# Kernel tuning notes

Hardware: AMD Instinct MI355X
Metric: run time of the kernel (lower is better)

## Reference

```python
import jax, jax.numpy as jnp
import numpy as np

N, DIN, DOUT, K, R = 4096, 256, 256, 3, 3
DENSITY = 0.005  # ~20 neighbors per node


def setup_inputs() -> dict:
    key = jax.random.key(0)
    ks = jax.random.split(key, 6)
    x = jax.random.normal(ks[0], (N, DIN), dtype=jnp.float32)
    supports = (jax.random.uniform(ks[1], (K, N, N)) < DENSITY).astype(jnp.int32)
    atten_supports = (jax.random.uniform(ks[2], (R, N, N)) < DENSITY).astype(jnp.int32)
    # torch Linear default init ~ U(-1/sqrt(fan_in), 1/sqrt(fan_in)); scaled normal is fine
    W_t = jax.random.normal(ks[3], (K, DIN, DOUT), dtype=jnp.float32) / np.sqrt(DIN).astype(np.float32)
    W_l = jax.random.normal(ks[4], (K, R + 1, DOUT), dtype=jnp.float32) / np.sqrt(DOUT).astype(np.float32)
    W_r = jax.random.normal(ks[5], (K, R + 1, DOUT), dtype=jnp.float32) / np.sqrt(DOUT).astype(np.float32)
    return {"x": x, "supports": supports, "atten_supports": atten_supports,
            "W_t": W_t, "W_l": W_l, "W_r": W_r}


def reference(x, supports, atten_supports, W_t, W_l, W_r):
    NEG = jnp.float32(-1e30)  # finite stand-in for -inf; exp(NEG - max) == 0 in fp32
    amask = (atten_supports != 0).astype(x.dtype)  # [R, N, N]
    out = None
    for k in range(K):
        wx = x @ W_t[k]                      # [N, Dout]
        al = wx @ W_l[k].T                   # [N, R+1] all left attention scalars
        ar = wx @ W_r[k].T                   # [N, R+1]
        # sum_i mask_i * (al_i[row] + ar_i[col]) without R dense [N,N] temps
        scores = (jnp.einsum('rnm,nr->nm', amask, al[:, :R])
                  + jnp.einsum('rnm,mr->nm', amask, ar[:, :R]))
        smask = (supports[k] != 0).astype(x.dtype)  # [N, N]
        scores = scores + smask * (al[:, R][:, None] + ar[:, R][None, :])
        # masked_fill(scores == 0, -inf) -> softmax -> NaN rows (no edges) -> 0
        valid = scores != 0
        probs = jax.nn.softmax(jnp.where(valid, scores, NEG), axis=-1)
        probs = jnp.where(valid.any(axis=-1, keepdims=True), probs, jnp.float32(0.0))
        out_k = probs @ wx                   # [N, Dout]
        out = out_k if out is None else out + out_k
    return jax.nn.elu(out)
```

## Files before the change

kernel.cpp:

```cpp
#include <hip/hip_runtime.h>
#include <hip/hip_bf16.h>
#include <math.h>

#define N 4096
#define DIN 256
#define DOUT 256
#define KK 3
#define CAP 512

typedef int i4 __attribute__((ext_vector_type(4)));

__global__ __launch_bounds__(256) void gemm_wx(const float* __restrict__ x,
                                               const float* __restrict__ Wt,
                                               float* __restrict__ wx) {
    __shared__ float As[16][68];
    __shared__ float Bs[16][68];
    const int k  = blockIdx.z;
    const int n0 = blockIdx.y * 64;
    const int d0 = blockIdx.x * 64;
    const int tx = threadIdx.x, ty = threadIdx.y;
    const int t  = ty * 16 + tx;
    float acc[4][4] = {};
    const float* xA = x + (size_t)(n0 + (t >> 2)) * DIN + ((t & 3) * 4);
    const float* wB = Wt + (size_t)k * DIN * DOUT + (size_t)(t >> 4) * DOUT + d0 + (t & 15) * 4;
    for (int k0 = 0; k0 < DIN; k0 += 16) {
        float4 xa = *(const float4*)(xA + k0);
        float4 wb = *(const float4*)(wB + (size_t)k0 * DOUT);
        const int r = t >> 2, c = (t & 3) * 4;
        As[c + 0][r] = xa.x; As[c + 1][r] = xa.y; As[c + 2][r] = xa.z; As[c + 3][r] = xa.w;
        *(float4*)&Bs[t >> 4][(t & 15) * 4] = wb;
        __syncthreads();
#pragma unroll
        for (int kk = 0; kk < 16; ++kk) {
            float4 a = *(const float4*)&As[kk][ty * 4];
            float4 b = *(const float4*)&Bs[kk][tx * 4];
            float av[4] = {a.x, a.y, a.z, a.w};
            float bv[4] = {b.x, b.y, b.z, b.w};
#pragma unroll
            for (int i = 0; i < 4; ++i)
#pragma unroll
                for (int j = 0; j < 4; ++j)
                    acc[i][j] = fmaf(av[i], bv[j], acc[i][j]);
        }
        __syncthreads();
    }
#pragma unroll
    for (int i = 0; i < 4; ++i) {
        const int row = n0 + ty * 4 + i;
        float4 o = {acc[i][0], acc[i][1], acc[i][2], acc[i][3]};
        *(float4*)(wx + ((size_t)k * N + row) * DOUT + d0 + tx * 4) = o;
    }
}

__global__ __launch_bounds__(256) void alar_kernel(const float* __restrict__ wx,
                                                   const float* __restrict__ Wl,
                                                   const float* __restrict__ Wr,
                                                   float* __restrict__ al,
                                                   float* __restrict__ ar) {
    const int k    = blockIdx.y;
    const int wid  = threadIdx.x >> 6;
    const int lane = threadIdx.x & 63;
    const int n    = blockIdx.x * 4 + wid;
    float4 wxv = *(const float4*)(wx + ((size_t)k * N + n) * DOUT + lane * 4);
#pragma unroll
    for (int j = 0; j < 4; ++j) {
        float4 wl = *(const float4*)(Wl + ((size_t)k * 4 + j) * DOUT + lane * 4);
        float4 wr = *(const float4*)(Wr + ((size_t)k * 4 + j) * DOUT + lane * 4);
        float pl = wxv.x * wl.x + wxv.y * wl.y + wxv.z * wl.z + wxv.w * wl.w;
        float pr = wxv.x * wr.x + wxv.y * wr.y + wxv.z * wr.z + wxv.w * wr.w;
#pragma unroll
        for (int o = 32; o > 0; o >>= 1) { pl += __shfl_xor(pl, o); pr += __shfl_xor(pr, o); }
        if (lane == 0) {
            al[((size_t)k * N + n) * 4 + j] = pl;
            ar[((size_t)k * N + n) * 4 + j] = pr;
        }
    }
}

__global__ __launch_bounds__(256) void build_kernel(const int* __restrict__ sup,
                                                    const int* __restrict__ att,
                                                    int* __restrict__ row_cnt,
                                                    unsigned int* __restrict__ entries) {
    const int n = blockIdx.x;
    __shared__ int scnt;
    if (threadIdx.x == 0) scnt = 0;
    __syncthreads();
    const int t = threadIdx.x;
#pragma unroll
    for (int i = 0; i < 4; ++i) {
        const int m0 = i * 1024 + t * 4;
        i4 a0 = __builtin_nontemporal_load((const i4*)(att + ((size_t)0 * N + n) * N + m0));
        i4 a1 = __builtin_nontemporal_load((const i4*)(att + ((size_t)1 * N + n) * N + m0));
        i4 a2 = __builtin_nontemporal_load((const i4*)(att + ((size_t)2 * N + n) * N + m0));
        i4 s0 = __builtin_nontemporal_load((const i4*)(sup + ((size_t)0 * N + n) * N + m0));
        i4 s1 = __builtin_nontemporal_load((const i4*)(sup + ((size_t)1 * N + n) * N + m0));
        i4 s2 = __builtin_nontemporal_load((const i4*)(sup + ((size_t)2 * N + n) * N + m0));
#pragma unroll
        for (int j = 0; j < 4; ++j) {
            unsigned bits = 0;
            if (a0[j]) bits |= 1u;
            if (a1[j]) bits |= 2u;
            if (a2[j]) bits |= 4u;
            if (s0[j]) bits |= 8u;
            if (s1[j]) bits |= 16u;
            if (s2[j]) bits |= 32u;
            if (bits) {
                int pos = atomicAdd(&scnt, 1);
                if (pos < CAP) entries[(size_t)n * CAP + pos] = (unsigned)(m0 + j) | (bits << 12);
            }
        }
    }
    __syncthreads();
    if (threadIdx.x == 0) row_cnt[n] = min(scnt, CAP);
}

__global__ __launch_bounds__(256) void attn_kernel(const float* __restrict__ wx,
                                                   const float* __restrict__ al,
                                                   const float* __restrict__ ar,
                                                   const int* __restrict__ row_cnt,
                                                   const unsigned int* __restrict__ entries,
                                                   float* __restrict__ out) {
    const int n = blockIdx.x;
    const int t = threadIdx.x;
    const int w = t >> 6;
    const int lane = t & 63;
    __shared__ unsigned int ent[CAP];
    __shared__ float sc[CAP];
    __shared__ float red[8];
    __shared__ float4 accbuf[4][64];
    const int cnt = row_cnt[n];
    for (int e = t; e < cnt; e += 256) ent[e] = entries[(size_t)n * CAP + e];
    __syncthreads();
    float4 acc4 = {0.f, 0.f, 0.f, 0.f};
    for (int k = 0; k < KK; ++k) {
        const float4 alv = *(const float4*)(al + ((size_t)k * N + n) * 4);
        const float* ark = ar + (size_t)k * N * 4;
        const unsigned kb = 8u << k;
        float lmax = -INFINITY;
        for (int e = t; e < cnt; e += 256) {
            const unsigned v = ent[e];
            const int m = v & 0xFFFu;
            const unsigned bits = v >> 12;
            float4 arv = *(const float4*)(ark + (size_t)m * 4);
            float s = 0.f;
            if (bits & 1u) s += alv.x + arv.x;
            if (bits & 2u) s += alv.y + arv.y;
            if (bits & 4u) s += alv.z + arv.z;
            if (bits & kb) s += alv.w + arv.w;
            sc[e] = s;
            if (s != 0.f) lmax = fmaxf(lmax, s);
        }
#pragma unroll
        for (int o = 32; o > 0; o >>= 1) lmax = fmaxf(lmax, __shfl_xor(lmax, o));
        if ((t & 63) == 0) red[t >> 6] = lmax;
        __syncthreads();
        const float rmax = fmaxf(fmaxf(red[0], red[1]), fmaxf(red[2], red[3]));
        __syncthreads();
        if (rmax != -INFINITY) {
            float lsum = 0.f;
            for (int e = t; e < cnt; e += 256) {
                const float s = sc[e];
                const float p = (s != 0.f) ? __expf(s - rmax) : 0.f;
                sc[e] = p;
                lsum += p;
            }
#pragma unroll
            for (int o = 32; o > 0; o >>= 1) lsum += __shfl_xor(lsum, o);
            if ((t & 63) == 0) red[t >> 6] = lsum;
            __syncthreads();
            const float inv = 1.f / (red[0] + red[1] + red[2] + red[3]);
            const float4* wxk4 = (const float4*)(wx + (size_t)k * N * DOUT) + lane;
            float4 pacc = {0.f, 0.f, 0.f, 0.f};
            int e = w;
            for (; e + 12 < cnt; e += 16) {
                const float p0 = sc[e], p1 = sc[e + 4], p2 = sc[e + 8], p3 = sc[e + 12];
                const int m0 = ent[e] & 0xFFF, m1 = ent[e + 4] & 0xFFF,
                          m2 = ent[e + 8] & 0xFFF, m3 = ent[e + 12] & 0xFFF;
                const float4 v0 = wxk4[(size_t)m0 * 64];
                const float4 v1 = wxk4[(size_t)m1 * 64];
                const float4 v2 = wxk4[(size_t)m2 * 64];
                const float4 v3 = wxk4[(size_t)m3 * 64];
                pacc.x = fmaf(p0, v0.x, pacc.x); pacc.y = fmaf(p0, v0.y, pacc.y);
                pacc.z = fmaf(p0, v0.z, pacc.z); pacc.w = fmaf(p0, v0.w, pacc.w);
                pacc.x = fmaf(p1, v1.x, pacc.x); pacc.y = fmaf(p1, v1.y, pacc.y);
                pacc.z = fmaf(p1, v1.z, pacc.z); pacc.w = fmaf(p1, v1.w, pacc.w);
                pacc.x = fmaf(p2, v2.x, pacc.x); pacc.y = fmaf(p2, v2.y, pacc.y);
                pacc.z = fmaf(p2, v2.z, pacc.z); pacc.w = fmaf(p2, v2.w, pacc.w);
                pacc.x = fmaf(p3, v3.x, pacc.x); pacc.y = fmaf(p3, v3.y, pacc.y);
                pacc.z = fmaf(p3, v3.z, pacc.z); pacc.w = fmaf(p3, v3.w, pacc.w);
            }
            for (; e < cnt; e += 4) {
                const float p = sc[e];
                const float4 v = wxk4[(size_t)(ent[e] & 0xFFF) * 64];
                pacc.x = fmaf(p, v.x, pacc.x); pacc.y = fmaf(p, v.y, pacc.y);
                pacc.z = fmaf(p, v.z, pacc.z); pacc.w = fmaf(p, v.w, pacc.w);
            }
            acc4.x = fmaf(inv, pacc.x, acc4.x);
            acc4.y = fmaf(inv, pacc.y, acc4.y);
            acc4.z = fmaf(inv, pacc.z, acc4.z);
            acc4.w = fmaf(inv, pacc.w, acc4.w);
            __syncthreads();
        }
    }
    accbuf[w][lane] = acc4;
    __syncthreads();
    if (t < 64) {
        const float4 s0 = accbuf[0][t], s1 = accbuf[1][t], s2 = accbuf[2][t], s3 = accbuf[3][t];
        float4 r;
        r.x = (s0.x + s1.x) + (s2.x + s3.x);
        r.y = (s0.y + s1.y) + (s2.y + s3.y);
        r.z = (s0.z + s1.z) + (s2.z + s3.z);
        r.w = (s0.w + s1.w) + (s2.w + s3.w);
        r.x = (r.x > 0.f) ? r.x : expm1f(r.x);
        r.y = (r.y > 0.f) ? r.y : expm1f(r.y);
        r.z = (r.z > 0.f) ? r.z : expm1f(r.z);
        r.w = (r.w > 0.f) ? r.w : expm1f(r.w);
        *(float4*)(out + (size_t)n * DOUT + t * 4) = r;
    }
}

extern "C" void kernel_launch(void* const* d_in, const int* in_sizes, int n_in,
                              void* d_out, int out_size, void* d_ws, size_t ws_size,
                              hipStream_t stream) {
    const float* x   = (const float*)d_in[0];
    const int*   sup = (const int*)d_in[1];
    const int*   att = (const int*)d_in[2];
    const float* Wt  = (const float*)d_in[3];
    const float* Wl  = (const float*)d_in[4];
    const float* Wr  = (const float*)d_in[5];
    float* out = (float*)d_out;

    char* ws = (char*)d_ws;
    float* wx        = (float*)(ws + 0);
    float* al        = (float*)(ws + 12582912);
    float* ar        = (float*)(ws + 12779520);
    int*   row_cnt   = (int*)  (ws + 12976128);
    unsigned int* entries = (unsigned int*)(ws + 12992512);

    gemm_wx<<<dim3(DOUT / 64, N / 64, KK), dim3(16, 16), 0, stream>>>(x, Wt, wx);
    alar_kernel<<<dim3(N / 4, KK), 256, 0, stream>>>(wx, Wl, Wr, al, ar);
    build_kernel<<<N, 256, 0, stream>>>(sup, att, row_cnt, entries);
    attn_kernel<<<N, 256, 0, stream>>>(wx, al, ar, row_cnt, entries, out);
}
```

Baseline: 526.3 us.

## Split attention per support into separate launches and compact nonzero-probability entries

Splits the attention kernel into one launch per support k, each accumulating into a workspace buffer, followed by a separate ELU finalize kernel. Within each launch, entries with nonzero scores are compacted into shared arrays via an atomic counter, so the gather over wx rows only visits entries valid for that k. The aim is to skip wx row loads for neighbors that belong to other supports and to improve L2 locality, since each launch touches only one k slice of wx. In exchange it adds three kernel launches, rereads the entry list three times, adds read-modify-write traffic on the accumulator, and makes summation order depend on atomic order.

```diff
diff --git a/kernel.cpp b/kernel.cpp
--- a/kernel.cpp
+++ b/kernel.cpp
@@ -114,93 +114,97 @@
     if (threadIdx.x == 0) row_cnt[n] = min(scnt, CAP);
 }
 
-__global__ __launch_bounds__(256) void attn_kernel(const float* __restrict__ wx,
-                                                   const float* __restrict__ al,
-                                                   const float* __restrict__ ar,
-                                                   const int* __restrict__ row_cnt,
-                                                   const unsigned int* __restrict__ entries,
-                                                   float* __restrict__ out) {
+__global__ __launch_bounds__(256) void attn_k(const float* __restrict__ wx,
+                                              const float* __restrict__ al,
+                                              const float* __restrict__ ar,
+                                              const int* __restrict__ row_cnt,
+                                              const unsigned int* __restrict__ entries,
+                                              float* __restrict__ out_acc,
+                                              int k) {
     const int n = blockIdx.x;
     const int t = threadIdx.x;
     const int w = t >> 6;
     const int lane = t & 63;
     __shared__ unsigned int ent[CAP];
     __shared__ float sc[CAP];
+    __shared__ unsigned short cent[CAP];
+    __shared__ float cp[CAP];
     __shared__ float red[8];
+    __shared__ int vcnt;
     __shared__ float4 accbuf[4][64];
     const int cnt = row_cnt[n];
     for (int e = t; e < cnt; e += 256) ent[e] = entries[(size_t)n * CAP + e];
     __syncthreads();
+    const float4 alv = *(const float4*)(al + ((size_t)k * N + n) * 4);
+    const float* ark = ar + (size_t)k * N * 4;
+    const unsigned kb = 8u << k;
+    float lmax = -INFINITY;
+    for (int e = t; e < cnt; e += 256) {
+        const unsigned v = ent[e];
+        const int m = v & 0xFFFu;
+        const unsigned bits = v >> 12;
+        float4 arv = *(const float4*)(ark + (size_t)m * 4);
+        float s = 0.f;
+        if (bits & 1u) s += alv.x + arv.x;
+        if (bits & 2u) s += alv.y + arv.y;
+        if (bits & 4u) s += alv.z + arv.z;
+        if (bits & kb) s += alv.w + arv.w;
+        sc[e] = s;
+        if (s != 0.f) lmax = fmaxf(lmax, s);
+    }
+#pragma unroll
+    for (int o = 32; o > 0; o >>= 1) lmax = fmaxf(lmax, __shfl_xor(lmax, o));
+    if (lane == 0) red[w] = lmax;
+    if (t == 0) vcnt = 0;
+    __syncthreads();
+    const float rmax = fmaxf(fmaxf(red[0], red[1]), fmaxf(red[2], red[3]));
+    __syncthreads();
     float4 acc4 = {0.f, 0.f, 0.f, 0.f};
-    for (int k = 0; k < KK; ++k) {
-        const float4 alv = *(const float4*)(al + ((size_t)k * N + n) * 4);
-        const float* ark = ar + (size_t)k * N * 4;
-        const unsigned kb = 8u << k;
-        float lmax = -INFINITY;
+    if (rmax != -INFINITY) {
+        float lsum = 0.f;
         for (int e = t; e < cnt; e += 256) {
-            const unsigned v = ent[e];
-            const int m = v & 0xFFFu;
-            const unsigned bits = v >> 12;
-            float4 arv = *(const float4*)(ark + (size_t)m * 4);
-            float s = 0.f;
-            if (bits & 1u) s += alv.x + arv.x;
-            if (bits & 2u) s += alv.y + arv.y;
-            if (bits & 4u) s += alv.z + arv.z;
-            if (bits & kb) s += alv.w + arv.w;
-            sc[e] = s;
-            if (s != 0.f) lmax = fmaxf(lmax, s);
-        }
-#pragma unroll
-        for (int o = 32; o > 0; o >>= 1) lmax = fmaxf(lmax, __shfl_xor(lmax, o));
-        if ((t & 63) == 0) red[t >> 6] = lmax;
-        __syncthreads();
-        const float rmax = fmaxf(fmaxf(red[0], red[1]), fmaxf(red[2], red[3]));
-        __syncthreads();
-        if (rmax != -INFINITY) {
-            float lsum = 0.f;
-            for (int e = t; e < cnt; e += 256) {
-                const float s = sc[e];
-                const float p = (s != 0.f) ? __expf(s - rmax) : 0.f;
-                sc[e] = p;
+            const float s = sc[e];
+            if (s != 0.f) {
+                const float p = __expf(s - rmax);
+                const int pos = atomicAdd(&vcnt, 1);
+                cent[pos] = (unsigned short)(ent[e] & 0xFFFu);
+                cp[pos] = p;
                 lsum += p;
             }
-#pragma unroll
-            for (int o = 32; o > 0; o >>= 1) lsum += __shfl_xor(lsum, o);
-            if ((t & 63) == 0) red[t >> 6] = lsum;
-            __syncthreads();
-            const float inv = 1.f / (red[0] + red[1] + red[2] + red[3]);
-            const float4* wxk4 = (const float4*)(wx + (size_t)k * N * DOUT) + lane;
-            float4 pacc = {0.f, 0.f, 0.f, 0.f};
-            int e = w;
-            for (; e + 12 < cnt; e += 16) {
-                const float p0 = sc[e], p1 = sc[e + 4], p2 = sc[e + 8], p3 = sc[e + 12];
-                const int m0 = ent[e] & 0xFFF, m1 = ent[e + 4] & 0xFFF,
-                          m2 = ent[e + 8] & 0xFFF, m3 = ent[e + 12] & 0xFFF;
-                const float4 v0 = wxk4[(size_t)m0 * 64];
-                const float4 v1 = wxk4[(size_t)m1 * 64];
-                const float4 v2 = wxk4[(size_t)m2 * 64];
-                const float4 v3 = wxk4[(size_t)m3 * 64];
-                pacc.x = fmaf(p0, v0.x, pacc.x); pacc.y = fmaf(p0, v0.y, pacc.y);
-                pacc.z = fmaf(p0, v0.z, pacc.z); pacc.w = fmaf(p0, v0.w, pacc.w);
-                pacc.x = fmaf(p1, v1.x, pacc.x); pacc.y = fmaf(p1, v1.y, pacc.y);
-                pacc.z = fmaf(p1, v1.z, pacc.z); pacc.w = fmaf(p1, v1.w, pacc.w);
-                pacc.x = fmaf(p2, v2.x, pacc.x); pacc.y = fmaf(p2, v2.y, pacc.y);
-                pacc.z = fmaf(p2, v2.z, pacc.z); pacc.w = fmaf(p2, v2.w, pacc.w);
-                pacc.x = fmaf(p3, v3.x, pacc.x); pacc.y = fmaf(p3, v3.y, pacc.y);
-                pacc.z = fmaf(p3, v3.z, pacc.z); pacc.w = fmaf(p3, v3.w, pacc.w);
-            }
-            for (; e < cnt; e += 4) {
-                const float p = sc[e];
-                const float4 v = wxk4[(size_t)(ent[e] & 0xFFF) * 64];
-                pacc.x = fmaf(p, v.x, pacc.x); pacc.y = fmaf(p, v.y, pacc.y);
-                pacc.z = fmaf(p, v.z, pacc.z); pacc.w = fmaf(p, v.w, pacc.w);
-            }
-            acc4.x = fmaf(inv, pacc.x, acc4.x);
-            acc4.y = fmaf(inv, pacc.y, acc4.y);
-            acc4.z = fmaf(inv, pacc.z, acc4.z);
-            acc4.w = fmaf(inv, pacc.w, acc4.w);
-            __syncthreads();
-        }
+        }
+#pragma unroll
+        for (int o = 32; o > 0; o >>= 1) lsum += __shfl_xor(lsum, o);
+        if (lane == 0) red[4 + w] = lsum;
+        __syncthreads();
+        const float inv = 1.f / (red[4] + red[5] + red[6] + red[7]);
+        const int vc = vcnt;
+        const float4* wxk4 = (const float4*)(wx + (size_t)k * N * DOUT) + lane;
+        float4 pacc = {0.f, 0.f, 0.f, 0.f};
+        int e = w;
+        for (; e + 12 < vc; e += 16) {
+            const float p0 = cp[e], p1 = cp[e + 4], p2 = cp[e + 8], p3 = cp[e + 12];
+            const int m0 = cent[e], m1 = cent[e + 4], m2 = cent[e + 8], m3 = cent[e + 12];
+            const float4 v0 = wxk4[(size_t)m0 * 64];
+            const float4 v1 = wxk4[(size_t)m1 * 64];
+            const float4 v2 = wxk4[(size_t)m2 * 64];
+            const float4 v3 = wxk4[(size_t)m3 * 64];
+            pacc.x = fmaf(p0, v0.x, pacc.x); pacc.y = fmaf(p0, v0.y, pacc.y);
+            pacc.z = fmaf(p0, v0.z, pacc.z); pacc.w = fmaf(p0, v0.w, pacc.w);
+            pacc.x = fmaf(p1, v1.x, pacc.x); pacc.y = fmaf(p1, v1.y, pacc.y);
+            pacc.z = fmaf(p1, v1.z, pacc.z); pacc.w = fmaf(p1, v1.w, pacc.w);
+            pacc.x = fmaf(p2, v2.x, pacc.x); pacc.y = fmaf(p2, v2.y, pacc.y);
+            pacc.z = fmaf(p2, v2.z, pacc.z); pacc.w = fmaf(p2, v2.w, pacc.w);
+            pacc.x = fmaf(p3, v3.x, pacc.x); pacc.y = fmaf(p3, v3.y, pacc.y);
+            pacc.z = fmaf(p3, v3.z, pacc.z); pacc.w = fmaf(p3, v3.w, pacc.w);
+        }
+        for (; e < vc; e += 4) {
+            const float p = cp[e];
+            const float4 v = wxk4[(size_t)cent[e] * 64];
+            pacc.x = fmaf(p, v.x, pacc.x); pacc.y = fmaf(p, v.y, pacc.y);
+            pacc.z = fmaf(p, v.z, pacc.z); pacc.w = fmaf(p, v.w, pacc.w);
+        }
+        acc4.x = inv * pacc.x; acc4.y = inv * pacc.y;
+        acc4.z = inv * pacc.z; acc4.w = inv * pacc.w;
     }
     accbuf[w][lane] = acc4;
     __syncthreads();
@@ -211,12 +215,26 @@
         r.y = (s0.y + s1.y) + (s2.y + s3.y);
         r.z = (s0.z + s1.z) + (s2.z + s3.z);
         r.w = (s0.w + s1.w) + (s2.w + s3.w);
-        r.x = (r.x > 0.f) ? r.x : expm1f(r.x);
-        r.y = (r.y > 0.f) ? r.y : expm1f(r.y);
-        r.z = (r.z > 0.f) ? r.z : expm1f(r.z);
-        r.w = (r.w > 0.f) ? r.w : expm1f(r.w);
-        *(float4*)(out + (size_t)n * DOUT + t * 4) = r;
-    }
+        float4* oa = (float4*)(out_acc + (size_t)n * DOUT) + t;
+        if (k == 0) {
+            *oa = r;
+        } else {
+            float4 old = *oa;
+            r.x += old.x; r.y += old.y; r.z += old.z; r.w += old.w;
+            *oa = r;
+        }
+    }
+}
+
+__global__ __launch_bounds__(256) void elu_finalize(const float* __restrict__ out_acc,
+                                                    float* __restrict__ out) {
+    const int i = blockIdx.x * 256 + threadIdx.x;
+    float4 v = ((const float4*)out_acc)[i];
+    v.x = (v.x > 0.f) ? v.x : expm1f(v.x);
+    v.y = (v.y > 0.f) ? v.y : expm1f(v.y);
+    v.z = (v.z > 0.f) ? v.z : expm1f(v.z);
+    v.w = (v.w > 0.f) ? v.w : expm1f(v.w);
+    ((float4*)out)[i] = v;
 }
 
 extern "C" void kernel_launch(void* const* d_in, const int* in_sizes, int n_in,
@@ -236,9 +254,12 @@
     float* ar        = (float*)(ws + 12779520);
     int*   row_cnt   = (int*)  (ws + 12976128);
     unsigned int* entries = (unsigned int*)(ws + 12992512);
+    float* out_acc   = (float*)(ws + 21381120);
 
     gemm_wx<<<dim3(DOUT / 64, N / 64, KK), dim3(16, 16), 0, stream>>>(x, Wt, wx);
     alar_kernel<<<dim3(N / 4, KK), 256, 0, stream>>>(wx, Wl, Wr, al, ar);
     build_kernel<<<N, 256, 0, stream>>>(sup, att, row_cnt, entries);
-    attn_kernel<<<N, 256, 0, stream>>>(wx, al, ar, row_cnt, entries, out);
-}
+    for (int k = 0; k < KK; ++k)
+        attn_k<<<N, 256, 0, stream>>>(wx, al, ar, row_cnt, entries, out_acc, k);
+    elu_finalize<<<N * DOUT / 1024, 256, 0, stream>>>(out_acc, out);
+}
```

After: 470.4 us. 1.12x faster.
